# Performance work log

Measured on AMD Instinct MI355X. Metric: run time of the kernel, lower is better.

## Reference

```python
import jax, jax.numpy as jnp
import numpy as np

N_EMBD = 768
N_HEAD = 12
B, T = 4, 2048


def setup_inputs() -> dict:
    key = jax.random.key(0)
    ks = jax.random.split(key, 9)
    D = N_EMBD
    s = 1.0 / np.sqrt(D)
    return {
        "x": jax.random.normal(ks[0], (B, T, D), dtype=jnp.float32),
        "Wq": jax.random.normal(ks[1], (D, D), dtype=jnp.float32) * s,
        "bq": jnp.zeros((D,), dtype=jnp.float32),
        "Wk": jax.random.normal(ks[2], (D, D), dtype=jnp.float32) * s,
        "bk": jnp.zeros((D,), dtype=jnp.float32),
        "Wv": jax.random.normal(ks[3], (D, D), dtype=jnp.float32) * s,
        "bv": jnp.zeros((D,), dtype=jnp.float32),
        "Wp": jax.random.normal(ks[4], (D, D), dtype=jnp.float32) * s,
        "bp": jnp.zeros((D,), dtype=jnp.float32),
    }


def reference(x, Wq, bq, Wk, bk, Wv, bv, Wp, bp):
    Bx, Tx, D = x.shape
    H = N_HEAD
    Dh = D // H
    # QKV projections (torch Linear: x @ W.T + b)
    q = (x @ Wq.T + bq).reshape(Bx, Tx, H, Dh).transpose(0, 2, 1, 3)  # [B,H,T,Dh]
    k = (x @ Wk.T + bk).reshape(Bx, Tx, H, Dh).transpose(0, 2, 1, 3)
    v = (x @ Wv.T + bv).reshape(Bx, Tx, H, Dh).transpose(0, 2, 1, 3)
    att = jnp.einsum("bhqd,bhkd->bhqk", q, k) / jnp.sqrt(jnp.float32(Dh))
    causal = jnp.tril(jnp.ones((Tx, Tx), dtype=bool))
    att = jnp.where(causal, att, jnp.float32(-1e9))
    att = jax.nn.softmax(att, axis=-1)  # attn_drop p=0 -> identity
    y = jnp.einsum("bhqk,bhkd->bhqd", att, v)
    y = y.transpose(0, 2, 1, 3).reshape(Bx, Tx, D)
    return y @ Wp.T + bp  # resid_drop p=0 -> identity
```

## Files before the change

kernel.cpp:

```cpp
#include <hip/hip_runtime.h>
#include <hip/hip_bf16.h>
#include <cstddef>

#define T_SEQ 2048
#define D_EMB 768
#define NHEAD 12
#define DH 64

typedef __attribute__((ext_vector_type(8))) short short8;
typedef __attribute__((ext_vector_type(4))) short short4v;
typedef __attribute__((ext_vector_type(4))) float floatx4;

__device__ __forceinline__ unsigned short f2bf(float f) {
    unsigned u = __float_as_uint(f);
    u = (u + 0x7FFFu + ((u >> 16) & 1u)) >> 16;
    return (unsigned short)u;
}

__device__ __forceinline__ void gload16(const void* g, void* l) {
    __builtin_amdgcn_global_load_lds(
        (const __attribute__((address_space(1))) void*)g,
        (__attribute__((address_space(3))) void*)l, 16, 0, 0);
}

__global__ __launch_bounds__(256)
void cast_bf16_kernel(const float* __restrict__ x,
                      const float* __restrict__ Wq, const float* __restrict__ Wk,
                      const float* __restrict__ Wv, const float* __restrict__ Wp,
                      __hip_bfloat16* __restrict__ xb,
                      __hip_bfloat16* __restrict__ wqkvb,
                      __hip_bfloat16* __restrict__ wpb)
{
    const int ci = blockIdx.x * 256 + threadIdx.x;
    const float* src;
    __hip_bfloat16* dst;
    size_t off;
    if (ci < 786432) {
        src = x; dst = xb; off = (size_t)ci * 8;
    } else {
        const int r  = ci - 786432;
        const int wi = r / 73728;
        const int ro = r - wi * 73728;
        off = (size_t)ro * 8;
        src = (wi == 0) ? Wq : (wi == 1) ? Wk : (wi == 2) ? Wv : Wp;
        dst = (wi < 3) ? wqkvb + (size_t)wi * 589824 : wpb;
    }
    const float4* s4 = reinterpret_cast<const float4*>(src + off);
    const float4 f0 = s4[0], f1 = s4[1];
    unsigned short us[8] = { f2bf(f0.x), f2bf(f0.y), f2bf(f0.z), f2bf(f0.w),
                             f2bf(f1.x), f2bf(f1.y), f2bf(f1.z), f2bf(f1.w) };
    *reinterpret_cast<short8*>(dst + off) = *reinterpret_cast<const short8*>(us);
}

template<int MODE>
__global__ __launch_bounds__(256)
void gemm_bf16_mfma(const __hip_bfloat16* __restrict__ A,
                    const __hip_bfloat16* __restrict__ Bm,
                    const float* __restrict__ b0, const float* __restrict__ b1,
                    const float* __restrict__ b2,
                    __hip_bfloat16* __restrict__ qo,
                    __hip_bfloat16* __restrict__ ko,
                    __hip_bfloat16* __restrict__ vo,
                    float* __restrict__ out)
{
    __shared__ __align__(16) __hip_bfloat16 As[128 * 64];
    __shared__ __align__(16) __hip_bfloat16 Bs[128 * 64];

    const int tid  = threadIdx.x;
    const int w    = tid >> 6, lane = tid & 63;
    const int g    = lane >> 4, c = lane & 15;
    const int m0   = blockIdx.x * 128, n0 = blockIdx.y * 128;
    const int wr   = w >> 1, wc = w & 1;
    const int srow = lane >> 3;
    const int scol = (lane & 7) * 8;

    floatx4 acc[4][4];
#pragma unroll
    for (int mi = 0; mi < 4; ++mi)
#pragma unroll
        for (int ni = 0; ni < 4; ++ni)
            acc[mi][ni] = (floatx4){0.f, 0.f, 0.f, 0.f};

    for (int kt = 0; kt < 12; ++kt) {
        const int k0 = kt * 64;
#pragma unroll
        for (int j = 0; j < 4; ++j) {
            const int ch = w * 4 + j;
            gload16(A  + (size_t)(m0 + ch * 8 + srow) * D_EMB + k0 + scol,
                    (char*)As + ch * 1024);
            gload16(Bm + (size_t)(n0 + ch * 8 + srow) * D_EMB + k0 + scol,
                    (char*)Bs + ch * 1024);
        }
        __syncthreads();
#pragma unroll
        for (int kk = 0; kk < 2; ++kk) {
            short8 af[4], bfr[4];
#pragma unroll
            for (int mi = 0; mi < 4; ++mi)
                af[mi] = *reinterpret_cast<const short8*>(
                    As + (wr * 64 + mi * 16 + c) * 64 + kk * 32 + g * 8);
#pragma unroll
            for (int ni = 0; ni < 4; ++ni)
                bfr[ni] = *reinterpret_cast<const short8*>(
                    Bs + (wc * 64 + ni * 16 + c) * 64 + kk * 32 + g * 8);
#pragma unroll
            for (int mi = 0; mi < 4; ++mi)
#pragma unroll
                for (int ni = 0; ni < 4; ++ni)
                    acc[mi][ni] = __builtin_amdgcn_mfma_f32_16x16x32_bf16(
                        af[mi], bfr[ni], acc[mi][ni], 0, 0, 0);
        }
        __syncthreads();
    }

    if (MODE == 0) {
        const int which = n0 / 768;
        const int nb    = n0 - which * 768 + wc * 64;
        const float* bias = (which == 0) ? b0 : (which == 1) ? b1 : b2;
        if (which < 2) {
            __hip_bfloat16* dst = (which == 0) ? qo : ko;
            const float scale = (which == 0) ? 0.125f : 1.0f;
#pragma unroll
            for (int mi = 0; mi < 4; ++mi) {
                const int m = m0 + wr * 64 + mi * 16 + 4 * g;
                const int b = m >> 11, t = m & 2047;
#pragma unroll
                for (int ni = 0; ni < 4; ++ni) {
                    const int n7 = nb + ni * 16 + c;
                    const int h = n7 >> 6, dh = n7 & 63;
                    const float bval = bias[n7];
                    const size_t base =
                        ((size_t)(b * NHEAD + h) * T_SEQ + t) * DH + dh;
#pragma unroll
                    for (int rr = 0; rr < 4; ++rr) {
                        unsigned short bits =
                            f2bf((acc[mi][ni][rr] + bval) * scale);
                        dst[base + (size_t)rr * DH] =
                            *reinterpret_cast<__hip_bfloat16*>(&bits);
                    }
                }
            }
        } else {
#pragma unroll
            for (int mi = 0; mi < 4; ++mi) {
                const int m = m0 + wr * 64 + mi * 16 + 4 * g;
                const int b = m >> 11, t = m & 2047;
#pragma unroll
                for (int ni = 0; ni < 4; ++ni) {
                    const int n7 = nb + ni * 16 + c;
                    const int h = n7 >> 6, dh = n7 & 63;
                    const float bval = bias[n7];
                    unsigned short us[4];
#pragma unroll
                    for (int rr = 0; rr < 4; ++rr)
                        us[rr] = f2bf(acc[mi][ni][rr] + bval);
                    *reinterpret_cast<short4v*>(
                        vo + ((size_t)(b * NHEAD + h) * DH + dh) * T_SEQ + t) =
                        *reinterpret_cast<const short4v*>(us);
                }
            }
        }
    } else {
#pragma unroll
        for (int mi = 0; mi < 4; ++mi) {
            const int m = m0 + wr * 64 + mi * 16 + 4 * g;
#pragma unroll
            for (int ni = 0; ni < 4; ++ni) {
                const int n = n0 + wc * 64 + ni * 16 + c;
                const float bval = b0[n];
#pragma unroll
                for (int rr = 0; rr < 4; ++rr)
                    out[(size_t)(m + rr) * D_EMB + n] = acc[mi][ni][rr] + bval;
            }
        }
    }
}

__global__ __launch_bounds__(256)
void attn_mfma_kernel(const __hip_bfloat16* __restrict__ qb,
                      const __hip_bfloat16* __restrict__ kbp,
                      const __hip_bfloat16* __restrict__ vtb,
                      __hip_bfloat16* __restrict__ y)
{
    __shared__ __align__(16) char Ksh[2][8192];
    __shared__ __align__(16) char Vsh[2][8192];
    __shared__ __align__(16) char Pbuf[4][2048];

    const int fid = blockIdx.x;
    const int xcd = fid & 7;
    const int ix  = fid >> 3;
    const int bh  = xcd * 6 + (ix >> 5);
    const int qt  = 31 - (ix & 31);

    const int w    = threadIdx.x >> 6;
    const int lane = threadIdx.x & 63;
    const int g    = lane >> 4;
    const int c    = lane & 15;
    const int q0   = qt * 64 + w * 16;

    const __hip_bfloat16* Qp = qb  + (size_t)bh * T_SEQ * DH;
    const char* Kg0 = (const char*)(kbp + (size_t)bh * T_SEQ * DH);
    const char* Vg0 = (const char*)(vtb + (size_t)bh * DH * T_SEQ);
    char* pw = Pbuf[w];

    short8 qf0 = *reinterpret_cast<const short8*>(Qp + (size_t)(q0 + c) * DH + 8 * g);
    short8 qf1 = *reinterpret_cast<const short8*>(Qp + (size_t)(q0 + c) * DH + 32 + 8 * g);

    floatx4 yacc[4];
#pragma unroll
    for (int n = 0; n < 4; ++n) yacc[n] = (floatx4){0.f, 0.f, 0.f, 0.f};
    float mrun[4], lsum[4];
#pragma unroll
    for (int r = 0; r < 4; ++r) { mrun[r] = -1e30f; lsum[r] = 0.f; }

    const int nkb = qt + 1;

    auto stage = [&](int buf, int kb0) {
        const char* Kg = Kg0 + (size_t)kb0 * 128;
        const char* Vg = Vg0 + (size_t)kb0 * 2;
#pragma unroll
        for (int i = 0; i < 2; ++i) {
            const int chb = i * 256 + w * 64;
            const int ch  = chb + lane;
            const int r   = ch >> 3;
            const int sg  = (ch & 7) ^ (r & 7);
            gload16(Kg + (size_t)r * 128  + sg * 16, Ksh[buf] + chb * 16);
            gload16(Vg + (size_t)r * 4096 + sg * 16, Vsh[buf] + chb * 16);
        }
    };

    stage(0, 0);
    __syncthreads();
    int cur = 0;

    for (int jb = 0; jb < nkb; ++jb) {
        if (jb + 1 < nkb) stage(cur ^ 1, (jb + 1) * 64);

        const char* Kb = Ksh[cur];
        const char* Vb = Vsh[cur];
        const int kb0 = jb * 64;

        floatx4 s[4];
#pragma unroll
        for (int n = 0; n < 4; ++n) s[n] = (floatx4){0.f, 0.f, 0.f, 0.f};
#pragma unroll
        for (int n = 0; n < 4; ++n) {
            const int rb = (16 * n + c) * 128;
            short8 kf0 = *reinterpret_cast<const short8*>(
                Kb + rb + ((g ^ (c & 7)) << 4));
            short8 kf1 = *reinterpret_cast<const short8*>(
                Kb + rb + (((4 + g) ^ (c & 7)) << 4));
            s[n] = __builtin_amdgcn_mfma_f32_16x16x32_bf16(qf0, kf0, s[n], 0, 0, 0);
            s[n] = __builtin_amdgcn_mfma_f32_16x16x32_bf16(qf1, kf1, s[n], 0, 0, 0);
        }

        if (jb == qt) {
#pragma unroll
            for (int n = 0; n < 4; ++n)
#pragma unroll
                for (int r = 0; r < 4; ++r)
                    if (kb0 + 16 * n + c > q0 + 4 * g + r) s[n][r] = -1e30f;
        }

        float mt[4];
#pragma unroll
        for (int r = 0; r < 4; ++r)
            mt[r] = fmaxf(fmaxf(s[0][r], s[1][r]), fmaxf(s[2][r], s[3][r]));
#pragma unroll
        for (int off = 8; off >= 1; off >>= 1)
#pragma unroll
            for (int r = 0; r < 4; ++r)
                mt[r] = fmaxf(mt[r], __shfl_xor(mt[r], off, 64));

        float corr[4];
#pragma unroll
        for (int r = 0; r < 4; ++r) {
            const float mn = fmaxf(mrun[r], mt[r]);
            corr[r] = __expf(mrun[r] - mn);
            mrun[r] = mn;
        }
#pragma unroll
        for (int n = 0; n < 4; ++n)
#pragma unroll
            for (int r = 0; r < 4; ++r) yacc[n][r] *= corr[r];

        float rs[4] = {0.f, 0.f, 0.f, 0.f};
#pragma unroll
        for (int n = 0; n < 4; ++n) {
            const int kf = n >> 1;
            const int gk = 2 * (n & 1) + (c >> 3);
            const int slot = gk ^ g;
#pragma unroll
            for (int r = 0; r < 4; ++r) {
                const float p = __expf(s[n][r] - mrun[r]);
                rs[r] += p;
                const int qrow = 4 * g + r;
                unsigned short bits = f2bf(p);
                *reinterpret_cast<unsigned short*>(
                    pw + kf * 1024 + qrow * 64 + (slot << 4) + (c & 7) * 2) = bits;
            }
        }
#pragma unroll
        for (int off = 8; off >= 1; off >>= 1)
#pragma unroll
            for (int r = 0; r < 4; ++r) rs[r] += __shfl_xor(rs[r], off, 64);
#pragma unroll
        for (int r = 0; r < 4; ++r) lsum[r] = lsum[r] * corr[r] + rs[r];

        asm volatile("s_waitcnt lgkmcnt(0)" ::: "memory");
        __builtin_amdgcn_sched_barrier(0);

        const int rslot = g ^ ((c >> 2) & 3);
        short8 pf0 = *reinterpret_cast<const short8*>(pw + c * 64 + (rslot << 4));
        short8 pf1 = *reinterpret_cast<const short8*>(pw + 1024 + c * 64 + (rslot << 4));

#pragma unroll
        for (int nd = 0; nd < 4; ++nd) {
            const int rb = (16 * nd + c) * 128;
            short8 vf0 = *reinterpret_cast<const short8*>(
                Vb + rb + ((g ^ (c & 7)) << 4));
            short8 vf1 = *reinterpret_cast<const short8*>(
                Vb + rb + (((4 + g) ^ (c & 7)) << 4));
            yacc[nd] = __builtin_amdgcn_mfma_f32_16x16x32_bf16(pf0, vf0, yacc[nd], 0, 0, 0);
            yacc[nd] = __builtin_amdgcn_mfma_f32_16x16x32_bf16(pf1, vf1, yacc[nd], 0, 0, 0);
        }

        __syncthreads();
        cur ^= 1;
    }

    const int b = bh / NHEAD, h = bh % NHEAD;
    float inv[4];
#pragma unroll
    for (int r = 0; r < 4; ++r) inv[r] = 1.f / lsum[r];
#pragma unroll
    for (int n = 0; n < 4; ++n)
#pragma unroll
        for (int r = 0; r < 4; ++r) {
            unsigned short bits = f2bf(yacc[n][r] * inv[r]);
            y[((size_t)b * T_SEQ + q0 + 4 * g + r) * D_EMB + h * DH + 16 * n + c] =
                *reinterpret_cast<__hip_bfloat16*>(&bits);
        }
}

extern "C" void kernel_launch(void* const* d_in, const int* in_sizes, int n_in,
                              void* d_out, int out_size, void* d_ws, size_t ws_size,
                              hipStream_t stream)
{
    const float* x  = (const float*)d_in[0];
    const float* Wq = (const float*)d_in[1];
    const float* bq = (const float*)d_in[2];
    const float* Wk = (const float*)d_in[3];
    const float* bk = (const float*)d_in[4];
    const float* Wv = (const float*)d_in[5];
    const float* bv = (const float*)d_in[6];
    const float* Wp = (const float*)d_in[7];
    const float* bp = (const float*)d_in[8];
    float* out = (float*)d_out;

    __hip_bfloat16* xb    = (__hip_bfloat16*)d_ws;
    __hip_bfloat16* wqkvb = xb + 6291456;
    __hip_bfloat16* wpb   = wqkvb + 1769472;
    __hip_bfloat16* qb    = wpb + 589824;
    __hip_bfloat16* kb    = qb + 6291456;
    __hip_bfloat16* vtb   = kb + 6291456;
    __hip_bfloat16* yb    = vtb + 6291456;

    cast_bf16_kernel<<<4224, 256, 0, stream>>>(x, Wq, Wk, Wv, Wp, xb, wqkvb, wpb);

    gemm_bf16_mfma<0><<<dim3(64, 18), 256, 0, stream>>>(
        xb, wqkvb, bq, bk, bv, qb, kb, vtb, nullptr);

    attn_mfma_kernel<<<1536, 256, 0, stream>>>(qb, kb, vtb, yb);

    gemm_bf16_mfma<1><<<dim3(64, 6), 256, 0, stream>>>(
        yb, wpb, bp, nullptr, nullptr, nullptr, nullptr, nullptr, out);
}
```

Baseline: 284.3 us.

## Double-buffer GEMM tiles, remap blocks per XCD, and process two query tiles per attention block

The GEMM now double-buffers its A/B shared tiles so the next K slice loads while the current one computes, and uses a 1D grid remapped so consecutive blocks on the same XCD share tiles. Each attention block now handles two 64-row query tiles (A and B) against one shared K/V stream, halving K/V staging per query. The P scratch buffer is padded to an 80-byte row stride to cut LDS bank conflicts. Softmax skips the rescale when the max grows by at most 8, and the row-sum reduction moves to the end. This costs more registers and shared memory per block, which may lower occupancy, and the lazy rescale depends on fp32 headroom.

```diff
diff --git a/kernel.cpp b/kernel.cpp
--- a/kernel.cpp
+++ b/kernel.cpp
@@ -63,13 +63,18 @@
                     __hip_bfloat16* __restrict__ vo,
                     float* __restrict__ out)
 {
-    __shared__ __align__(16) __hip_bfloat16 As[128 * 64];
-    __shared__ __align__(16) __hip_bfloat16 Bs[128 * 64];
+    __shared__ __align__(16) __hip_bfloat16 As[2][128 * 64];
+    __shared__ __align__(16) __hip_bfloat16 Bs[2][128 * 64];
+
+    const int fid = blockIdx.x;
+    const int lin = (MODE == 0) ? ((fid & 7) * 144 + (fid >> 3))
+                                : ((fid & 7) * 48  + (fid >> 3));
+    const int m0 = (lin & 63) * 128;
+    const int n0 = (lin >> 6) * 128;
 
     const int tid  = threadIdx.x;
     const int w    = tid >> 6, lane = tid & 63;
     const int g    = lane >> 4, c = lane & 15;
-    const int m0   = blockIdx.x * 128, n0 = blockIdx.y * 128;
     const int wr   = w >> 1, wc = w & 1;
     const int srow = lane >> 3;
     const int scol = (lane & 7) * 8;
@@ -81,28 +86,34 @@
         for (int ni = 0; ni < 4; ++ni)
             acc[mi][ni] = (floatx4){0.f, 0.f, 0.f, 0.f};
 
-    for (int kt = 0; kt < 12; ++kt) {
-        const int k0 = kt * 64;
+    auto stage = [&](int buf, int k0) {
 #pragma unroll
         for (int j = 0; j < 4; ++j) {
             const int ch = w * 4 + j;
             gload16(A  + (size_t)(m0 + ch * 8 + srow) * D_EMB + k0 + scol,
-                    (char*)As + ch * 1024);
+                    (char*)As[buf] + ch * 1024);
             gload16(Bm + (size_t)(n0 + ch * 8 + srow) * D_EMB + k0 + scol,
-                    (char*)Bs + ch * 1024);
-        }
-        __syncthreads();
+                    (char*)Bs[buf] + ch * 1024);
+        }
+    };
+
+    stage(0, 0);
+    __syncthreads();
+    int cur = 0;
+
+    for (int kt = 0; kt < 12; ++kt) {
+        if (kt + 1 < 12) stage(cur ^ 1, (kt + 1) * 64);
 #pragma unroll
         for (int kk = 0; kk < 2; ++kk) {
             short8 af[4], bfr[4];
 #pragma unroll
             for (int mi = 0; mi < 4; ++mi)
                 af[mi] = *reinterpret_cast<const short8*>(
-                    As + (wr * 64 + mi * 16 + c) * 64 + kk * 32 + g * 8);
+                    As[cur] + (wr * 64 + mi * 16 + c) * 64 + kk * 32 + g * 8);
 #pragma unroll
             for (int ni = 0; ni < 4; ++ni)
                 bfr[ni] = *reinterpret_cast<const short8*>(
-                    Bs + (wc * 64 + ni * 16 + c) * 64 + kk * 32 + g * 8);
+                    Bs[cur] + (wc * 64 + ni * 16 + c) * 64 + kk * 32 + g * 8);
 #pragma unroll
             for (int mi = 0; mi < 4; ++mi)
 #pragma unroll
@@ -111,6 +122,7 @@
                         af[mi], bfr[ni], acc[mi][ni], 0, 0, 0);
         }
         __syncthreads();
+        cur ^= 1;
     }
 
     if (MODE == 0) {
@@ -184,36 +196,43 @@
 {
     __shared__ __align__(16) char Ksh[2][8192];
     __shared__ __align__(16) char Vsh[2][8192];
-    __shared__ __align__(16) char Pbuf[4][2048];
+    __shared__ __align__(16) char Pbuf[4][2][2560];
 
     const int fid = blockIdx.x;
     const int xcd = fid & 7;
     const int ix  = fid >> 3;
-    const int bh  = xcd * 6 + (ix >> 5);
-    const int qt  = 31 - (ix & 31);
+    const int bh  = xcd * 6 + (ix >> 4);
+    const int qt  = 15 - (ix & 15);
 
     const int w    = threadIdx.x >> 6;
     const int lane = threadIdx.x & 63;
     const int g    = lane >> 4;
     const int c    = lane & 15;
-    const int q0   = qt * 64 + w * 16;
+    const int q0A  = qt * 128 + w * 16;
+    const int q0B  = q0A + 64;
 
     const __hip_bfloat16* Qp = qb  + (size_t)bh * T_SEQ * DH;
     const char* Kg0 = (const char*)(kbp + (size_t)bh * T_SEQ * DH);
     const char* Vg0 = (const char*)(vtb + (size_t)bh * DH * T_SEQ);
-    char* pw = Pbuf[w];
-
-    short8 qf0 = *reinterpret_cast<const short8*>(Qp + (size_t)(q0 + c) * DH + 8 * g);
-    short8 qf1 = *reinterpret_cast<const short8*>(Qp + (size_t)(q0 + c) * DH + 32 + 8 * g);
-
-    floatx4 yacc[4];
-#pragma unroll
-    for (int n = 0; n < 4; ++n) yacc[n] = (floatx4){0.f, 0.f, 0.f, 0.f};
-    float mrun[4], lsum[4];
-#pragma unroll
-    for (int r = 0; r < 4; ++r) { mrun[r] = -1e30f; lsum[r] = 0.f; }
-
-    const int nkb = qt + 1;
+    char* pwA = Pbuf[w][0];
+    char* pwB = Pbuf[w][1];
+
+    short8 qfA0 = *reinterpret_cast<const short8*>(Qp + (size_t)(q0A + c) * DH + 8 * g);
+    short8 qfA1 = *reinterpret_cast<const short8*>(Qp + (size_t)(q0A + c) * DH + 32 + 8 * g);
+    short8 qfB0 = *reinterpret_cast<const short8*>(Qp + (size_t)(q0B + c) * DH + 8 * g);
+    short8 qfB1 = *reinterpret_cast<const short8*>(Qp + (size_t)(q0B + c) * DH + 32 + 8 * g);
+
+    floatx4 yA[4], yB[4];
+#pragma unroll
+    for (int n = 0; n < 4; ++n) {
+        yA[n] = (floatx4){0.f, 0.f, 0.f, 0.f};
+        yB[n] = (floatx4){0.f, 0.f, 0.f, 0.f};
+    }
+    float mA[4], mB[4], lA[4], lB[4];
+#pragma unroll
+    for (int r = 0; r < 4; ++r) { mA[r] = -1e30f; mB[r] = -1e30f; lA[r] = 0.f; lB[r] = 0.f; }
+
+    const int nkb = 2 * qt + 2;
 
     auto stage = [&](int buf, int kb0) {
         const char* Kg = Kg0 + (size_t)kb0 * 128;
@@ -229,6 +248,50 @@
         }
     };
 
+    auto softmax_set = [&](floatx4* s, float* mrun, float* lsum, floatx4* yacc,
+                           char* pws) {
+        float mt[4];
+#pragma unroll
+        for (int r = 0; r < 4; ++r)
+            mt[r] = fmaxf(fmaxf(s[0][r], s[1][r]), fmaxf(s[2][r], s[3][r]));
+#pragma unroll
+        for (int off = 8; off >= 1; off >>= 1)
+#pragma unroll
+            for (int r = 0; r < 4; ++r)
+                mt[r] = fmaxf(mt[r], __shfl_xor(mt[r], off, 64));
+
+        float gmax = mt[0] - mrun[0];
+#pragma unroll
+        for (int r = 1; r < 4; ++r) gmax = fmaxf(gmax, mt[r] - mrun[r]);
+        if (!__all(gmax <= 8.0f)) {
+            float corr[4];
+#pragma unroll
+            for (int r = 0; r < 4; ++r) {
+                const float mn = fmaxf(mrun[r], mt[r]);
+                corr[r] = __expf(mrun[r] - mn);
+                mrun[r] = mn;
+                lsum[r] *= corr[r];
+            }
+#pragma unroll
+            for (int n = 0; n < 4; ++n)
+#pragma unroll
+                for (int r = 0; r < 4; ++r) yacc[n][r] *= corr[r];
+        }
+#pragma unroll
+        for (int n = 0; n < 4; ++n) {
+            const int kf   = n >> 1;
+            const int slot = (2 * (n & 1) + (c >> 3)) ^ g;
+#pragma unroll
+            for (int r = 0; r < 4; ++r) {
+                const float p = __expf(s[n][r] - mrun[r]);
+                lsum[r] += p;
+                unsigned short bits = f2bf(p);
+                *reinterpret_cast<unsigned short*>(
+                    pws + kf * 1280 + (4 * g + r) * 80 + (slot << 4) + (c & 7) * 2) = bits;
+            }
+        }
+    };
+
     stage(0, 0);
     __syncthreads();
     int cur = 0;
@@ -238,108 +301,111 @@
 
         const char* Kb = Ksh[cur];
         const char* Vb = Vsh[cur];
-        const int kb0 = jb * 64;
-
-        floatx4 s[4];
-#pragma unroll
-        for (int n = 0; n < 4; ++n) s[n] = (floatx4){0.f, 0.f, 0.f, 0.f};
+        const int kb0  = jb * 64;
+        const bool actA = (jb <= 2 * qt);
+
+        short8 kf0[4], kf1[4];
 #pragma unroll
         for (int n = 0; n < 4; ++n) {
             const int rb = (16 * n + c) * 128;
-            short8 kf0 = *reinterpret_cast<const short8*>(
-                Kb + rb + ((g ^ (c & 7)) << 4));
-            short8 kf1 = *reinterpret_cast<const short8*>(
-                Kb + rb + (((4 + g) ^ (c & 7)) << 4));
-            s[n] = __builtin_amdgcn_mfma_f32_16x16x32_bf16(qf0, kf0, s[n], 0, 0, 0);
-            s[n] = __builtin_amdgcn_mfma_f32_16x16x32_bf16(qf1, kf1, s[n], 0, 0, 0);
-        }
-
-        if (jb == qt) {
+            kf0[n] = *reinterpret_cast<const short8*>(Kb + rb + ((g ^ (c & 7)) << 4));
+            kf1[n] = *reinterpret_cast<const short8*>(Kb + rb + (((4 + g) ^ (c & 7)) << 4));
+        }
+
+        floatx4 sA[4], sB[4];
+#pragma unroll
+        for (int n = 0; n < 4; ++n) {
+            sA[n] = (floatx4){0.f, 0.f, 0.f, 0.f};
+            sB[n] = (floatx4){0.f, 0.f, 0.f, 0.f};
+        }
+        if (actA) {
+#pragma unroll
+            for (int n = 0; n < 4; ++n) {
+                sA[n] = __builtin_amdgcn_mfma_f32_16x16x32_bf16(qfA0, kf0[n], sA[n], 0, 0, 0);
+                sA[n] = __builtin_amdgcn_mfma_f32_16x16x32_bf16(qfA1, kf1[n], sA[n], 0, 0, 0);
+            }
+        }
+#pragma unroll
+        for (int n = 0; n < 4; ++n) {
+            sB[n] = __builtin_amdgcn_mfma_f32_16x16x32_bf16(qfB0, kf0[n], sB[n], 0, 0, 0);
+            sB[n] = __builtin_amdgcn_mfma_f32_16x16x32_bf16(qfB1, kf1[n], sB[n], 0, 0, 0);
+        }
+
+        if (actA && jb == 2 * qt) {
 #pragma unroll
             for (int n = 0; n < 4; ++n)
 #pragma unroll
                 for (int r = 0; r < 4; ++r)
-                    if (kb0 + 16 * n + c > q0 + 4 * g + r) s[n][r] = -1e30f;
-        }
-
-        float mt[4];
-#pragma unroll
-        for (int r = 0; r < 4; ++r)
-            mt[r] = fmaxf(fmaxf(s[0][r], s[1][r]), fmaxf(s[2][r], s[3][r]));
-#pragma unroll
-        for (int off = 8; off >= 1; off >>= 1)
-#pragma unroll
-            for (int r = 0; r < 4; ++r)
-                mt[r] = fmaxf(mt[r], __shfl_xor(mt[r], off, 64));
-
-        float corr[4];
-#pragma unroll
-        for (int r = 0; r < 4; ++r) {
-            const float mn = fmaxf(mrun[r], mt[r]);
-            corr[r] = __expf(mrun[r] - mn);
-            mrun[r] = mn;
-        }
-#pragma unroll
-        for (int n = 0; n < 4; ++n)
-#pragma unroll
-            for (int r = 0; r < 4; ++r) yacc[n][r] *= corr[r];
-
-        float rs[4] = {0.f, 0.f, 0.f, 0.f};
-#pragma unroll
-        for (int n = 0; n < 4; ++n) {
-            const int kf = n >> 1;
-            const int gk = 2 * (n & 1) + (c >> 3);
-            const int slot = gk ^ g;
-#pragma unroll
-            for (int r = 0; r < 4; ++r) {
-                const float p = __expf(s[n][r] - mrun[r]);
-                rs[r] += p;
-                const int qrow = 4 * g + r;
-                unsigned short bits = f2bf(p);
-                *reinterpret_cast<unsigned short*>(
-                    pw + kf * 1024 + qrow * 64 + (slot << 4) + (c & 7) * 2) = bits;
-            }
-        }
-#pragma unroll
-        for (int off = 8; off >= 1; off >>= 1)
-#pragma unroll
-            for (int r = 0; r < 4; ++r) rs[r] += __shfl_xor(rs[r], off, 64);
-#pragma unroll
-        for (int r = 0; r < 4; ++r) lsum[r] = lsum[r] * corr[r] + rs[r];
+                    if (kb0 + 16 * n + c > q0A + 4 * g + r) sA[n][r] = -1e30f;
+        }
+        if (jb == nkb - 1) {
+#pragma unroll
+            for (int n = 0; n < 4; ++n)
+#pragma unroll
+                for (int r = 0; r < 4; ++r)
+                    if (kb0 + 16 * n + c > q0B + 4 * g + r) sB[n][r] = -1e30f;
+        }
+
+        if (actA) softmax_set(sA, mA, lA, yA, pwA);
+        softmax_set(sB, mB, lB, yB, pwB);
 
         asm volatile("s_waitcnt lgkmcnt(0)" ::: "memory");
         __builtin_amdgcn_sched_barrier(0);
 
+        short8 vf0[4], vf1[4];
+#pragma unroll
+        for (int n = 0; n < 4; ++n) {
+            const int rb = (16 * n + c) * 128;
+            vf0[n] = *reinterpret_cast<const short8*>(Vb + rb + ((g ^ (c & 7)) << 4));
+            vf1[n] = *reinterpret_cast<const short8*>(Vb + rb + (((4 + g) ^ (c & 7)) << 4));
+        }
+
         const int rslot = g ^ ((c >> 2) & 3);
-        short8 pf0 = *reinterpret_cast<const short8*>(pw + c * 64 + (rslot << 4));
-        short8 pf1 = *reinterpret_cast<const short8*>(pw + 1024 + c * 64 + (rslot << 4));
-
-#pragma unroll
-        for (int nd = 0; nd < 4; ++nd) {
-            const int rb = (16 * nd + c) * 128;
-            short8 vf0 = *reinterpret_cast<const short8*>(
-                Vb + rb + ((g ^ (c & 7)) << 4));
-            short8 vf1 = *reinterpret_cast<const short8*>(
-                Vb + rb + (((4 + g) ^ (c & 7)) << 4));
-            yacc[nd] = __builtin_amdgcn_mfma_f32_16x16x32_bf16(pf0, vf0, yacc[nd], 0, 0, 0);
-            yacc[nd] = __builtin_amdgcn_mfma_f32_16x16x32_bf16(pf1, vf1, yacc[nd], 0, 0, 0);
+        if (actA) {
+            short8 pf0 = *reinterpret_cast<const short8*>(pwA + c * 80 + (rslot << 4));
+            short8 pf1 = *reinterpret_cast<const short8*>(pwA + 1280 + c * 80 + (rslot << 4));
+#pragma unroll
+            for (int nd = 0; nd < 4; ++nd) {
+                yA[nd] = __builtin_amdgcn_mfma_f32_16x16x32_bf16(pf0, vf0[nd], yA[nd], 0, 0, 0);
+                yA[nd] = __builtin_amdgcn_mfma_f32_16x16x32_bf16(pf1, vf1[nd], yA[nd], 0, 0, 0);
+            }
+        }
+        {
+            short8 pf0 = *reinterpret_cast<const short8*>(pwB + c * 80 + (rslot << 4));
+            short8 pf1 = *reinterpret_cast<const short8*>(pwB + 1280 + c * 80 + (rslot << 4));
+#pragma unroll
+            for (int nd = 0; nd < 4; ++nd) {
+                yB[nd] = __builtin_amdgcn_mfma_f32_16x16x32_bf16(pf0, vf0[nd], yB[nd], 0, 0, 0);
+                yB[nd] = __builtin_amdgcn_mfma_f32_16x16x32_bf16(pf1, vf1[nd], yB[nd], 0, 0, 0);
+            }
         }
 
         __syncthreads();
         cur ^= 1;
     }
 
+#pragma unroll
+    for (int off = 8; off >= 1; off >>= 1)
+#pragma unroll
+        for (int r = 0; r < 4; ++r) {
+            lA[r] += __shfl_xor(lA[r], off, 64);
+            lB[r] += __shfl_xor(lB[r], off, 64);
+        }
+
     const int b = bh / NHEAD, h = bh % NHEAD;
-    float inv[4];
-#pragma unroll
-    for (int r = 0; r < 4; ++r) inv[r] = 1.f / lsum[r];
+    float iA[4], iB[4];
+#pragma unroll
+    for (int r = 0; r < 4; ++r) { iA[r] = 1.f / lA[r]; iB[r] = 1.f / lB[r]; }
 #pragma unroll
     for (int n = 0; n < 4; ++n)
 #pragma unroll
         for (int r = 0; r < 4; ++r) {
-            unsigned short bits = f2bf(yacc[n][r] * inv[r]);
-            y[((size_t)b * T_SEQ + q0 + 4 * g + r) * D_EMB + h * DH + 16 * n + c] =
-                *reinterpret_cast<__hip_bfloat16*>(&bits);
+            unsigned short ba = f2bf(yA[n][r] * iA[r]);
+            unsigned short bb = f2bf(yB[n][r] * iB[r]);
+            y[((size_t)b * T_SEQ + q0A + 4 * g + r) * D_EMB + h * DH + 16 * n + c] =
+                *reinterpret_cast<__hip_bfloat16*>(&ba);
+            y[((size_t)b * T_SEQ + q0B + 4 * g + r) * D_EMB + h * DH + 16 * n + c] =
+                *reinterpret_cast<__hip_bfloat16*>(&bb);
         }
 }
 
@@ -368,11 +434,11 @@
 
     cast_bf16_kernel<<<4224, 256, 0, stream>>>(x, Wq, Wk, Wv, Wp, xb, wqkvb, wpb);
 
-    gemm_bf16_mfma<0><<<dim3(64, 18), 256, 0, stream>>>(
+    gemm_bf16_mfma<0><<<1152, 256, 0, stream>>>(
         xb, wqkvb, bq, bk, bv, qb, kb, vtb, nullptr);
 
-    attn_mfma_kernel<<<1536, 256, 0, stream>>>(qb, kb, vtb, yb);
-
-    gemm_bf16_mfma<1><<<dim3(64, 6), 256, 0, stream>>>(
+    attn_mfma_kernel<<<768, 256, 0, stream>>>(qb, kb, vtb, yb);
+
+    gemm_bf16_mfma<1><<<384, 256, 0, stream>>>(
         yb, wpb, bp, nullptr, nullptr, nullptr, nullptr, nullptr, out);
 }
```

New measurement: 302.3 us. +6.3%, slower.
